# Kernel tuning notes

Hardware: AMD Instinct MI355X
Metric: run time of the kernel (lower is better)

The kernel has to match this reference:

```python
import jax, jax.numpy as jnp
import numpy as np
import math

D_MODEL = 1024
N_HEAD = 16
FFN_HIDDEN = 4096
EPS = 1e-12


def _layernorm(x, gamma, beta):
    # faithful to repo: unbiased std (ddof=1), divide by (std + eps)
    mean = jnp.mean(x, axis=-1, keepdims=True)
    std = jnp.std(x, axis=-1, keepdims=True, ddof=1)
    return gamma * ((x - mean) / (std + EPS)) + beta


def setup_inputs() -> dict:
    key = jax.random.key(0)
    ks = jax.random.split(key, 12)
    B, L, D, H = 2, 2048, D_MODEL, FFN_HIDDEN
    s = 0.02
    inp = {
        "x": jax.random.normal(ks[0], (B, L, D), dtype=jnp.float32),
        "src_mask": jnp.ones((B, 1, 1, L), dtype=jnp.int32),
        "wq_w": jax.random.normal(ks[1], (D, D), jnp.float32) * s,
        "wq_b": jnp.zeros((D,), jnp.float32),
        "wk_w": jax.random.normal(ks[2], (D, D), jnp.float32) * s,
        "wk_b": jnp.zeros((D,), jnp.float32),
        "wv_w": jax.random.normal(ks[3], (D, D), jnp.float32) * s,
        "wv_b": jnp.zeros((D,), jnp.float32),
        "wo_w": jax.random.normal(ks[4], (D, D), jnp.float32) * s,
        "wo_b": jnp.zeros((D,), jnp.float32),
        "gamma1": jnp.ones((D,), jnp.float32),
        "beta1": jnp.zeros((D,), jnp.float32),
        "ff1_w": jax.random.normal(ks[5], (D, H), jnp.float32) * s,
        "ff1_b": jnp.zeros((H,), jnp.float32),
        "ff2_w": jax.random.normal(ks[6], (H, D), jnp.float32) * s,
        "ff2_b": jnp.zeros((D,), jnp.float32),
        "gamma2": jnp.ones((D,), jnp.float32),
        "beta2": jnp.zeros((D,), jnp.float32),
    }
    return inp


def _encoder_layer(x, src_mask, wq_w, wq_b, wk_w, wk_b, wv_w, wv_b, wo_w, wo_b,
                   gamma1, beta1, ff1_w, ff1_b, ff2_w, ff2_b, gamma2, beta2):
    B, L, D = x.shape
    H = N_HEAD
    d_t = D // H
    # projections
    q = x @ wq_w + wq_b
    k = x @ wk_w + wk_b
    v = x @ wv_w + wv_b
    # faithful .view() split: reshape [B,L,D] -> [B,H,L,d_t] (no transpose)
    q = q.reshape(B, H, L, d_t)
    k = k.reshape(B, H, L, d_t)
    v = v.reshape(B, H, L, d_t)
    score = jnp.einsum("bhqd,bhkd->bhqk", q, k) / math.sqrt(d_t)
    score = jnp.where(src_mask == 0, jnp.float32(-1e-12), score)
    score = jax.nn.softmax(score, axis=-1)
    out = jnp.einsum("bhqk,bhkd->bhqd", score, v)
    out = out.reshape(B, L, D)  # faithful .view() concat
    attn = out @ wo_w + wo_b
    # residual + LN1 (dropout p=0)
    x1 = _layernorm(attn + x, gamma1, beta1)
    # FFN
    ff = jax.nn.relu(x1 @ ff1_w + ff1_b) @ ff2_w + ff2_b
    return _layernorm(ff + x1, gamma2, beta2)


def reference(x, src_mask, wq_w, wq_b, wk_w, wk_b, wv_w, wv_b, wo_w, wo_b,
              gamma1, beta1, ff1_w, ff1_b, ff2_w, ff2_b, gamma2, beta2):
    return _encoder_layer(x, src_mask, wq_w, wq_b, wk_w, wk_b, wv_w, wv_b,
                          wo_w, wo_b, gamma1, beta1, ff1_w, ff1_b, ff2_w,
                          ff2_b, gamma2, beta2)
```

## Files before the change

### kernel.cpp

```cpp
#include <hip/hip_runtime.h>
#include <hip/hip_bf16.h>
#include <cstdint>
#include <cstddef>

using bf16 = __hip_bfloat16;
typedef __attribute__((ext_vector_type(8))) short short8v;
typedef __attribute__((ext_vector_type(4))) short short4v;
typedef __attribute__((ext_vector_type(4))) float float4v;

__device__ inline float b2f(short s) {
  union { float f; uint32_t u; } z; z.u = ((uint32_t)(uint16_t)s) << 16; return z.f;
}
__device__ inline short f2b(float f) {
  bf16 h = __float2bfloat16(f);
  return *reinterpret_cast<short*>(&h);
}

typedef const __attribute__((address_space(1))) uint32_t* gas1p;
typedef __attribute__((address_space(3))) uint32_t* las3p;
__device__ inline void gload_lds16(const void* g, void* l) {
  __builtin_amdgcn_global_load_lds((gas1p)g, (las3p)l, 16, 0, 0);
}

__device__ inline void xcd_swizzle(int& bx, int& by, int& bz) {
  const int gx = gridDim.x, gy = gridDim.y;
  const int nwg = gx * gy * gridDim.z;
  const int wgid = blockIdx.x + gx * (blockIdx.y + gy * blockIdx.z);
  const int swz = (wgid & 7) * (nwg >> 3) + (wgid >> 3);
  bx = swz % gx;
  by = (swz / gx) % gy;
  bz = swz / (gx * gy);
}

__global__ __launch_bounds__(512, 2) void gemm_bt256(
    const bf16* __restrict__ A, const bf16* __restrict__ Bt,
    const float* __restrict__ bias, void* __restrict__ C,
    int K, int ldc, int relu_mode, int out_f32) {
  __shared__ __align__(16) bf16 As[256 * 32];
  __shared__ __align__(16) bf16 Bs[256 * 32];
  const int tid = threadIdx.x;
  const int w = tid >> 6, lane = tid & 63;
  const int quad = lane >> 4, l16 = lane & 15;
  const int wrow = (w >> 2) * 128, wcol = (w & 3) * 64;
  const int mbase = blockIdx.y * 256, nbase = blockIdx.x * 256;
  const int row0 = tid >> 2, p0 = tid & 3;
  const int row1 = (tid + 512) >> 2, p1 = (tid + 512) & 3;

  float4v acc[8][4];
#pragma unroll
  for (int i = 0; i < 8; i++)
#pragma unroll
    for (int j = 0; j < 4; j++) acc[i][j] = (float4v){0.f, 0.f, 0.f, 0.f};

  for (int k0 = 0; k0 < K; k0 += 32) {
    __syncthreads();
    gload_lds16(A + (size_t)(mbase + row0) * K + k0 + p0 * 8, (char*)As + w * 1024);
    gload_lds16(A + (size_t)(mbase + row1) * K + k0 + p1 * 8, (char*)As + 8192 + w * 1024);
    gload_lds16(Bt + (size_t)(nbase + row0) * K + k0 + p0 * 8, (char*)Bs + w * 1024);
    gload_lds16(Bt + (size_t)(nbase + row1) * K + k0 + p1 * 8, (char*)Bs + 8192 + w * 1024);
    __syncthreads();

    short8v a[8], b[4];
#pragma unroll
    for (int mt = 0; mt < 8; mt++)
      a[mt] = *reinterpret_cast<const short8v*>(As + (wrow + mt * 16 + l16) * 32 + quad * 8);
#pragma unroll
    for (int nt = 0; nt < 4; nt++)
      b[nt] = *reinterpret_cast<const short8v*>(Bs + (wcol + nt * 16 + l16) * 32 + quad * 8);
#pragma unroll
    for (int mt = 0; mt < 8; mt++)
#pragma unroll
      for (int nt = 0; nt < 4; nt++)
        acc[mt][nt] = __builtin_amdgcn_mfma_f32_16x16x32_bf16(a[mt], b[nt], acc[mt][nt], 0, 0, 0);
  }

#pragma unroll
  for (int nt = 0; nt < 4; nt++) {
    int col = nbase + wcol + nt * 16 + l16;
    float bv = bias[col];
#pragma unroll
    for (int mt = 0; mt < 8; mt++) {
      int row = mbase + wrow + mt * 16 + quad * 4;
#pragma unroll
      for (int r = 0; r < 4; r++) {
        float v = acc[mt][nt][r] + bv;
        if (relu_mode) v = fmaxf(v, 0.f);
        size_t idx = (size_t)(row + r) * ldc + col;
        if (out_f32) ((float*)C)[idx] = v;
        else         ((short*)C)[idx] = f2b(v);
      }
    }
  }
}

__global__ __launch_bounds__(256) void gemm_pipe(
    const bf16* __restrict__ A, const bf16* __restrict__ Bt,
    float* __restrict__ C, int K, int ldc, int k_len) {
  __shared__ __align__(16) bf16 As[2][2][128 * 32];
  __shared__ __align__(16) bf16 Bs[2][2][128 * 32];
  const int tid = threadIdx.x;
  const int w = tid >> 6, lane = tid & 63;
  const int quad = lane >> 4, l16 = lane & 15;
  const int wrow = (w >> 1) * 64, wcol = (w & 1) * 64;
  int bx, by, bz;
  xcd_swizzle(bx, by, bz);
  const int mbase = by * 128, nbase = bx * 128;
  const int c0 = w * 128 + lane;
  const int row0 = c0 >> 2, p0 = c0 & 3;
  const int row1 = (c0 + 64) >> 2, p1 = (c0 + 64) & 3;
  const int kbase = bz * k_len;

  const bf16* ag0 = A + (size_t)(mbase + row0) * K + kbase + p0 * 8;
  const bf16* ag1 = A + (size_t)(mbase + row1) * K + kbase + p1 * 8;
  const bf16* bg0 = Bt + (size_t)(nbase + row0) * K + kbase + p0 * 8;
  const bf16* bg1 = Bt + (size_t)(nbase + row1) * K + kbase + p1 * 8;

  auto stage = [&](int t64, int bi) {
    const int ko = t64 * 64;
#pragma unroll
    for (int h = 0; h < 2; h++) {
      char* da = (char*)As + (size_t)(bi * 2 + h) * 8192 + w * 2048;
      char* db = (char*)Bs + (size_t)(bi * 2 + h) * 8192 + w * 2048;
      gload_lds16(ag0 + ko + h * 32, da);
      gload_lds16(ag1 + ko + h * 32, da + 1024);
      gload_lds16(bg0 + ko + h * 32, db);
      gload_lds16(bg1 + ko + h * 32, db + 1024);
    }
  };

  float4v acc[4][4];
  for (int i = 0; i < 4; i++)
    for (int j = 0; j < 4; j++) acc[i][j] = (float4v){0.f, 0.f, 0.f, 0.f};

  const int KT2 = k_len >> 6;
  stage(0, 0);
  __syncthreads();

  for (int kt = 0; kt < KT2; kt++) {
    const int pb = kt & 1;
    if (kt + 1 < KT2) stage(kt + 1, 1 - pb);

#pragma unroll
    for (int h = 0; h < 2; h++) {
      const bf16* Ah = &As[pb][h][0];
      const bf16* Bh = &Bs[pb][h][0];
      short8v a[4], b[4];
      for (int mt = 0; mt < 4; mt++)
        a[mt] = *reinterpret_cast<const short8v*>(Ah + (wrow + mt * 16 + l16) * 32 + quad * 8);
      for (int nt = 0; nt < 4; nt++)
        b[nt] = *reinterpret_cast<const short8v*>(Bh + (wcol + nt * 16 + l16) * 32 + quad * 8);
      for (int mt = 0; mt < 4; mt++)
        for (int nt = 0; nt < 4; nt++)
          acc[mt][nt] = __builtin_amdgcn_mfma_f32_16x16x32_bf16(a[mt], b[nt], acc[mt][nt], 0, 0, 0);
    }

    __syncthreads();
  }

  for (int nt = 0; nt < 4; nt++) {
    int col = nbase + wcol + nt * 16 + l16;
    for (int mt = 0; mt < 4; mt++) {
      int row = mbase + wrow + mt * 16 + quad * 4;
      for (int r = 0; r < 4; r++)
        atomicAdd(&C[(size_t)(row + r) * ldc + col], acc[mt][nt][r]);
    }
  }
}

__global__ __launch_bounds__(256) void bias_init(
    const float* __restrict__ bias, float* __restrict__ C) {
  int c = threadIdx.x * 4;
  float4 bv = *reinterpret_cast<const float4*>(bias + c);
  *reinterpret_cast<float4*>(C + (size_t)blockIdx.x * 1024 + c) = bv;
}

__global__ __launch_bounds__(256) void attn_kernel(
    const bf16* __restrict__ qkv, const int* __restrict__ mask,
    bf16* __restrict__ ao) {
  __shared__ __align__(16) short Vt[2][64 * 72];
  __shared__ __align__(16) short Ks[2][64 * 64];

  const int tid = threadIdx.x;
  const int w = tid >> 6, lane = tid & 63;
  const int quad = lane >> 4, l16 = lane & 15;
  const int bh = blockIdx.y, b = bh >> 4;
  const int row0 = bh * 128;
  const int qbase = blockIdx.x * 128 + w * 32;
  const int kvp = tid & 15, dg = tid >> 4;
  const int krow = tid >> 3, kc = tid & 7;

  short8v aq[2][2];
  for (int h = 0; h < 2; h++)
    for (int dh = 0; dh < 2; dh++) {
      int local = (qbase + h * 16 + l16) * 64 + dh * 32 + quad * 8;
      aq[h][dh] = *reinterpret_cast<const short8v*>(
          qkv + (size_t)(row0 + (local >> 10)) * 3072 + (local & 1023));
    }

  const bf16* pks0;
  {
    int local = krow * 64 + kc * 8;
    pks0 = qkv + (size_t)(row0 + (local >> 10)) * 3072 + (local & 1023) + 1024;
  }
  const bf16* pks1 = pks0 + 6144;
  const bf16* pva;
  const bf16* pvb;
  {
    int la = (2 * kvp) * 64 + dg * 4;
    pva = qkv + (size_t)(row0 + (la >> 10)) * 3072 + (la & 1023) + 2048;
    int lb = (2 * kvp + 1) * 64 + dg * 4;
    pvb = qkv + (size_t)(row0 + (lb >> 10)) * 3072 + (lb & 1023) + 2048;
  }
  const bf16* pva2 = pva + 6144;
  const bf16* pvb2 = pvb + 6144;
  const int* pm = mask + b * 2048 + quad * 4;

  float4v o[2][4];
  for (int h = 0; h < 2; h++)
    for (int nt = 0; nt < 4; nt++) o[h][nt] = (float4v){0.f, 0.f, 0.f, 0.f};
  float4v lacc[2];
  lacc[0] = (float4v){0.f, 0.f, 0.f, 0.f};
  lacc[1] = (float4v){0.f, 0.f, 0.f, 0.f};
  short8v vone;
  for (int j = 0; j < 8; j++) vone[j] = (short)0x3F80;

  short8v kr0, kr1;
  short4v va, vb, va2, vb2;
  kr0 = *reinterpret_cast<const short8v*>(pks0);
  kr1 = *reinterpret_cast<const short8v*>(pks1);
  va  = *reinterpret_cast<const short4v*>(pva);
  vb  = *reinterpret_cast<const short4v*>(pvb);
  va2 = *reinterpret_cast<const short4v*>(pva2);
  vb2 = *reinterpret_cast<const short4v*>(pvb2);
  int4 mc0 = *reinterpret_cast<const int4*>(pm);
  int4 mc1 = *reinterpret_cast<const int4*>(pm + 16);
  int4 mc2 = *reinterpret_cast<const int4*>(pm + 32);
  int4 mc3 = *reinterpret_cast<const int4*>(pm + 48);
  pks0 += 12288; pks1 += 12288; pva += 12288; pvb += 12288;
  pva2 += 12288; pvb2 += 12288; pm += 64;
  {
    const int sw = (kc ^ (krow & 7)) << 3;
    *reinterpret_cast<short8v*>(&Ks[0][krow * 64 + sw]) = kr0;
    *reinterpret_cast<short8v*>(&Ks[0][(krow + 32) * 64 + sw]) = kr1;
    uint32_t* vt = reinterpret_cast<uint32_t*>(&Vt[0][0]);
    for (int i = 0; i < 4; i++) {
      vt[(dg * 4 + i) * 36 + kvp] =
          ((uint32_t)(uint16_t)vb[i] << 16) | (uint16_t)(uint16_t)va[i];
      vt[(dg * 4 + i) * 36 + 16 + kvp] =
          ((uint32_t)(uint16_t)vb2[i] << 16) | (uint16_t)(uint16_t)va2[i];
    }
  }
  __syncthreads();

  for (int it = 0; it < 32; it++) {
    const int pb = it & 1;
    short8v knr0, knr1;
    short4v vna, vnb, vna2, vnb2;
    int4 mn0, mn1, mn2, mn3;
    if (it < 31) {
      knr0 = *reinterpret_cast<const short8v*>(pks0);
      knr1 = *reinterpret_cast<const short8v*>(pks1);
      vna  = *reinterpret_cast<const short4v*>(pva);
      vnb  = *reinterpret_cast<const short4v*>(pvb);
      vna2 = *reinterpret_cast<const short4v*>(pva2);
      vnb2 = *reinterpret_cast<const short4v*>(pvb2);
      mn0 = *reinterpret_cast<const int4*>(pm);
      mn1 = *reinterpret_cast<const int4*>(pm + 16);
      mn2 = *reinterpret_cast<const int4*>(pm + 32);
      mn3 = *reinterpret_cast<const int4*>(pm + 48);
      pks0 += 12288; pks1 += 12288; pva += 12288; pvb += 12288;
      pva2 += 12288; pvb2 += 12288; pm += 64;
    }

#pragma unroll
    for (int sub = 0; sub < 2; sub++) {
      short8v kc_[2][2];
      for (int s = 0; s < 2; s++)
        for (int dh = 0; dh < 2; dh++) {
          int rr = sub * 32 + s * 16 + l16;
          kc_[s][dh] = *reinterpret_cast<const short8v*>(
              &Ks[pb][rr * 64 + (((dh * 4 + quad) ^ (l16 & 7)) << 3)]);
        }

      float4v st[2][2];
      for (int s = 0; s < 2; s++)
        for (int h = 0; h < 2; h++) {
          float4v t = (float4v){0.f, 0.f, 0.f, 0.f};
          t = __builtin_amdgcn_mfma_f32_16x16x32_bf16(kc_[s][0], aq[h][0], t, 0, 0, 0);
          t = __builtin_amdgcn_mfma_f32_16x16x32_bf16(kc_[s][1], aq[h][1], t, 0, 0, 0);
          st[s][h] = t;
        }

      short8v pf[2];
      for (int h = 0; h < 2; h++) {
        float ev[2][4];
        for (int s = 0; s < 2; s++) {
          int4 mv = sub ? (s ? mc3 : mc2) : (s ? mc1 : mc0);
          int mm[4] = {mv.x, mv.y, mv.z, mv.w};
          for (int r = 0; r < 4; r++) {
            float y = st[s][h][r];
            y = (mm[r] == 0) ? -1.4427e-12f : y;
            ev[s][r] = __builtin_amdgcn_exp2f(y);
          }
        }
        uint32_t a0, a1, b0, b1;
        asm("v_cvt_pk_bf16_f32 %0, %1, %2" : "=v"(a0) : "v"(ev[0][0]), "v"(ev[0][1]));
        asm("v_cvt_pk_bf16_f32 %0, %1, %2" : "=v"(a1) : "v"(ev[0][2]), "v"(ev[0][3]));
        asm("v_cvt_pk_bf16_f32 %0, %1, %2" : "=v"(b0) : "v"(ev[1][0]), "v"(ev[1][1]));
        asm("v_cvt_pk_bf16_f32 %0, %1, %2" : "=v"(b1) : "v"(ev[1][2]), "v"(ev[1][3]));
        asm("v_permlane32_swap_b32 %0, %1" : "+v"(b0), "+v"(a0));
        asm("v_permlane16_swap_b32 %0, %1" : "+v"(b0), "+v"(a0));
        asm("v_permlane32_swap_b32 %0, %1" : "+v"(b1), "+v"(a1));
        asm("v_permlane16_swap_b32 %0, %1" : "+v"(b1), "+v"(a1));
        union { short8v s8; uint32_t u[4]; } pfu;
        pfu.u[0] = a0; pfu.u[1] = a1; pfu.u[2] = b0; pfu.u[3] = b1;
        pf[h] = pfu.s8;
      }

      for (int h = 0; h < 2; h++)
        lacc[h] = __builtin_amdgcn_mfma_f32_16x16x32_bf16(pf[h], vone, lacc[h], 0, 0, 0);
      for (int nt = 0; nt < 4; nt++) {
        short8v bv = *reinterpret_cast<const short8v*>(
            &Vt[pb][(nt * 16 + l16) * 72 + sub * 32 + quad * 8]);
        for (int h = 0; h < 2; h++)
          o[h][nt] = __builtin_amdgcn_mfma_f32_16x16x32_bf16(pf[h], bv, o[h][nt], 0, 0, 0);
      }
    }

    if (it < 31) {
      const int sw = (kc ^ (krow & 7)) << 3;
      *reinterpret_cast<short8v*>(&Ks[1 - pb][krow * 64 + sw]) = knr0;
      *reinterpret_cast<short8v*>(&Ks[1 - pb][(krow + 32) * 64 + sw]) = knr1;
      uint32_t* vt = reinterpret_cast<uint32_t*>(&Vt[1 - pb][0]);
      for (int i = 0; i < 4; i++) {
        vt[(dg * 4 + i) * 36 + kvp] =
            ((uint32_t)(uint16_t)vnb[i] << 16) | (uint16_t)(uint16_t)vna[i];
        vt[(dg * 4 + i) * 36 + 16 + kvp] =
            ((uint32_t)(uint16_t)vnb2[i] << 16) | (uint16_t)(uint16_t)vna2[i];
      }
      mc0 = mn0; mc1 = mn1; mc2 = mn2; mc3 = mn3;
    }
    __syncthreads();
  }

  for (int h = 0; h < 2; h++)
    for (int r = 0; r < 4; r++) {
      float linv = 1.0f / lacc[h][r];
      int qg = qbase + h * 16 + quad * 4 + r;
      for (int nt = 0; nt < 4; nt++) {
        int d = nt * 16 + l16;
        ao[(size_t)bh * 131072 + (size_t)qg * 64 + d] = __float2bfloat16(o[h][nt][r] * linv);
      }
    }
}

__global__ __launch_bounds__(256) void ln_resid(
    const void* __restrict__ a, const void* __restrict__ xres,
    const float* __restrict__ gamma, const float* __restrict__ beta,
    void* __restrict__ out, int a_f32, int x_f32, int out_f32) {
  __shared__ float red[8];
  const int row = blockIdx.x, tid = threadIdx.x;
  const int w = tid >> 6, lane = tid & 63;
  const size_t base = (size_t)row * 1024;
  float v[4]; float sum = 0.f, ss = 0.f;
  for (int i = 0; i < 4; i++) {
    int c = tid + i * 256;
    float av = a_f32 ? ((const float*)a)[base + c] : b2f(((const short*)a)[base + c]);
    float xv = x_f32 ? ((const float*)xres)[base + c] : b2f(((const short*)xres)[base + c]);
    v[i] = av + xv;
    sum += v[i]; ss += v[i] * v[i];
  }
  for (int off = 1; off < 64; off <<= 1) {
    sum += __shfl_xor(sum, off);
    ss  += __shfl_xor(ss, off);
  }
  if (lane == 0) { red[w * 2] = sum; red[w * 2 + 1] = ss; }
  __syncthreads();
  sum = red[0] + red[2] + red[4] + red[6];
  ss  = red[1] + red[3] + red[5] + red[7];
  float mean = sum * (1.0f / 1024.0f);
  float var = (ss - 1024.0f * mean * mean) * (1.0f / 1023.0f);
  var = fmaxf(var, 0.f);
  float rden = 1.0f / (sqrtf(var) + 1e-12f);
  for (int i = 0; i < 4; i++) {
    int c = tid + i * 256;
    float y = gamma[c] * ((v[i] - mean) * rden) + beta[c];
    if (out_f32) ((float*)out)[base + c] = y;
    else         ((short*)out)[base + c] = f2b(y);
  }
}

__global__ __launch_bounds__(256) void transpose_k(
    const float* __restrict__ in, bf16* __restrict__ out, int R, int C,
    float scale) {
  __shared__ short t[32][33];
  const int tx = threadIdx.x, ty = threadIdx.y;
  const int cb = blockIdx.x * 32, rb = blockIdx.y * 32;
  for (int j = 0; j < 4; j++)
    t[ty + j * 8][tx] = f2b(in[(size_t)(rb + ty + j * 8) * C + cb + tx] * scale);
  __syncthreads();
  for (int j = 0; j < 4; j++)
    ((short*)out)[(size_t)(cb + ty + j * 8) * R + rb + tx] = t[tx][ty + j * 8];
}

__global__ __launch_bounds__(256) void concat3(
    const float* __restrict__ a, const float* __restrict__ b,
    const float* __restrict__ c, float* __restrict__ out) {
  int i = blockIdx.x * 256 + threadIdx.x;
  float v;
  if (i < 1024)       v = a[i] * 0.18033688f;
  else if (i < 2048)  v = b[i - 1024];
  else                v = c[i - 2048];
  out[i] = v;
}

__global__ __launch_bounds__(256) void cast_f32_bf16(
    const float* __restrict__ in, bf16* __restrict__ out) {
  int i0 = (blockIdx.x * 256 + threadIdx.x) * 4;
  float4 f = *reinterpret_cast<const float4*>(in + i0);
  short* o = (short*)out + i0;
  o[0] = f2b(f.x); o[1] = f2b(f.y); o[2] = f2b(f.z); o[3] = f2b(f.w);
}

extern "C" void kernel_launch(void* const* d_in, const int* in_sizes, int n_in,
                              void* d_out, int out_size, void* d_ws, size_t ws_size,
                              hipStream_t stream) {
  (void)in_sizes; (void)n_in; (void)out_size; (void)ws_size;
  const float* x    = (const float*)d_in[0];
  const int*   mask = (const int*)d_in[1];
  const float* wq_w = (const float*)d_in[2];
  const float* wq_b = (const float*)d_in[3];
  const float* wk_w = (const float*)d_in[4];
  const float* wk_b = (const float*)d_in[5];
  const float* wv_w = (const float*)d_in[6];
  const float* wv_b = (const float*)d_in[7];
  const float* wo_w = (const float*)d_in[8];
  const float* wo_b = (const float*)d_in[9];
  const float* g1   = (const float*)d_in[10];
  const float* be1  = (const float*)d_in[11];
  const float* f1w  = (const float*)d_in[12];
  const float* f1b  = (const float*)d_in[13];
  const float* f2w  = (const float*)d_in[14];
  const float* f2b_ = (const float*)d_in[15];
  const float* g2   = (const float*)d_in[16];
  const float* be2  = (const float*)d_in[17];
  float* out = (float*)d_out;
  char* ws = (char*)d_ws;

  bf16*  QKV  = (bf16*)(ws + 0);
  bf16*  Xbf  = (bf16*)(ws + 25165824);
  bf16*  AO   = (bf16*)(ws + 25165824);
  float* PROJ = (float*)(ws + 0);
  bf16*  H    = (bf16*)(ws + 0);
  bf16*  X1   = (bf16*)(ws + 33554432);
  bf16*  WT   = (bf16*)(ws + 41943040);
  float* BQKV = (float*)(ws + 48234496);

  const float QSCALE = 0.18033688f;

  dim3 tb(32, 8);
  cast_f32_bf16<<<dim3(4096), dim3(256), 0, stream>>>(x, Xbf);
  transpose_k<<<dim3(32, 32), tb, 0, stream>>>(wq_w, WT, 1024, 1024, QSCALE);
  transpose_k<<<dim3(32, 32), tb, 0, stream>>>(wk_w, WT + 1024 * 1024, 1024, 1024, 1.0f);
  transpose_k<<<dim3(32, 32), tb, 0, stream>>>(wv_w, WT + 2 * 1024 * 1024, 1024, 1024, 1.0f);
  concat3<<<dim3(12), dim3(256), 0, stream>>>(wq_b, wk_b, wv_b, BQKV);
  gemm_bt256<<<dim3(12, 16), dim3(512), 0, stream>>>(Xbf, WT, BQKV, QKV, 1024, 3072, 0, 0);
  attn_kernel<<<dim3(16, 32), dim3(256), 0, stream>>>(QKV, mask, AO);
  transpose_k<<<dim3(32, 32), tb, 0, stream>>>(wo_w, WT, 1024, 1024, 1.0f);
  bias_init<<<dim3(4096), dim3(256), 0, stream>>>(wo_b, PROJ);
  gemm_pipe<<<dim3(8, 32, 2), dim3(256), 0, stream>>>(AO, WT, PROJ, 1024, 1024, 512);
  ln_resid<<<dim3(4096), dim3(256), 0, stream>>>(PROJ, x, g1, be1, X1, 1, 1, 0);
  transpose_k<<<dim3(128, 32), tb, 0, stream>>>(f1w, WT, 1024, 4096, 1.0f);
  gemm_bt256<<<dim3(16, 16), dim3(512), 0, stream>>>(X1, WT, f1b, H, 1024, 4096, 1, 0);
  transpose_k<<<dim3(32, 128), tb, 0, stream>>>(f2w, WT, 4096, 1024, 1.0f);
  bias_init<<<dim3(4096), dim3(256), 0, stream>>>(f2b_, out);
  gemm_pipe<<<dim3(8, 32, 2), dim3(256), 0, stream>>>(H, WT, out, 4096, 1024, 2048);
  ln_resid<<<dim3(4096), dim3(256), 0, stream>>>(out, X1, g2, be2, out, 1, 0, 1);
}
```

Measured before the change: 432.6 us.

## Double-buffer GEMM LDS tiles with K=64 stages to overlap loads and MFMA

The 256x256 GEMM kernel now uses two LDS buffers, each holding a 64-wide K slab split into two 32-wide halves. It prefetches the next slab with global_load_lds while computing on the current one, and needs one barrier per 64 K instead of two per 32 K. LDS use grows from 32KB to 128KB per block, which may cap occupancy below the declared 2 blocks per CU. The code also assumes K is a multiple of 64.

```diff
diff --git a/kernel.cpp b/kernel.cpp
--- a/kernel.cpp
+++ b/kernel.cpp
@@ -36,8 +36,8 @@
     const bf16* __restrict__ A, const bf16* __restrict__ Bt,
     const float* __restrict__ bias, void* __restrict__ C,
     int K, int ldc, int relu_mode, int out_f32) {
-  __shared__ __align__(16) bf16 As[256 * 32];
-  __shared__ __align__(16) bf16 Bs[256 * 32];
+  __shared__ __align__(16) bf16 As[2][2][256 * 32];
+  __shared__ __align__(16) bf16 Bs[2][2][256 * 32];
   const int tid = threadIdx.x;
   const int w = tid >> 6, lane = tid & 63;
   const int quad = lane >> 4, l16 = lane & 15;
@@ -46,32 +46,57 @@
   const int row0 = tid >> 2, p0 = tid & 3;
   const int row1 = (tid + 512) >> 2, p1 = (tid + 512) & 3;
 
+  const bf16* ag0 = A + (size_t)(mbase + row0) * K + p0 * 8;
+  const bf16* ag1 = A + (size_t)(mbase + row1) * K + p1 * 8;
+  const bf16* bg0 = Bt + (size_t)(nbase + row0) * K + p0 * 8;
+  const bf16* bg1 = Bt + (size_t)(nbase + row1) * K + p1 * 8;
+
+  auto stage = [&](int t64, int bi) {
+    const int ko = t64 * 64;
+#pragma unroll
+    for (int h = 0; h < 2; h++) {
+      char* da = (char*)As + (size_t)(bi * 2 + h) * 16384 + w * 1024;
+      char* db = (char*)Bs + (size_t)(bi * 2 + h) * 16384 + w * 1024;
+      gload_lds16(ag0 + ko + h * 32, da);
+      gload_lds16(ag1 + ko + h * 32, da + 8192);
+      gload_lds16(bg0 + ko + h * 32, db);
+      gload_lds16(bg1 + ko + h * 32, db + 8192);
+    }
+  };
+
   float4v acc[8][4];
 #pragma unroll
   for (int i = 0; i < 8; i++)
 #pragma unroll
     for (int j = 0; j < 4; j++) acc[i][j] = (float4v){0.f, 0.f, 0.f, 0.f};
 
-  for (int k0 = 0; k0 < K; k0 += 32) {
+  const int KT2 = K >> 6;
+  stage(0, 0);
+  __syncthreads();
+
+  for (int kt = 0; kt < KT2; kt++) {
+    const int pb = kt & 1;
+    if (kt + 1 < KT2) stage(kt + 1, 1 - pb);
+
+#pragma unroll
+    for (int h = 0; h < 2; h++) {
+      const bf16* Ah = &As[pb][h][0];
+      const bf16* Bh = &Bs[pb][h][0];
+      short8v a[8], b[4];
+#pragma unroll
+      for (int mt = 0; mt < 8; mt++)
+        a[mt] = *reinterpret_cast<const short8v*>(Ah + (wrow + mt * 16 + l16) * 32 + quad * 8);
+#pragma unroll
+      for (int nt = 0; nt < 4; nt++)
+        b[nt] = *reinterpret_cast<const short8v*>(Bh + (wcol + nt * 16 + l16) * 32 + quad * 8);
+#pragma unroll
+      for (int mt = 0; mt < 8; mt++)
+#pragma unroll
+        for (int nt = 0; nt < 4; nt++)
+          acc[mt][nt] = __builtin_amdgcn_mfma_f32_16x16x32_bf16(a[mt], b[nt], acc[mt][nt], 0, 0, 0);
+    }
+
     __syncthreads();
-    gload_lds16(A + (size_t)(mbase + row0) * K + k0 + p0 * 8, (char*)As + w * 1024);
-    gload_lds16(A + (size_t)(mbase + row1) * K + k0 + p1 * 8, (char*)As + 8192 + w * 1024);
-    gload_lds16(Bt + (size_t)(nbase + row0) * K + k0 + p0 * 8, (char*)Bs + w * 1024);
-    gload_lds16(Bt + (size_t)(nbase + row1) * K + k0 + p1 * 8, (char*)Bs + 8192 + w * 1024);
-    __syncthreads();
-
-    short8v a[8], b[4];
-#pragma unroll
-    for (int mt = 0; mt < 8; mt++)
-      a[mt] = *reinterpret_cast<const short8v*>(As + (wrow + mt * 16 + l16) * 32 + quad * 8);
-#pragma unroll
-    for (int nt = 0; nt < 4; nt++)
-      b[nt] = *reinterpret_cast<const short8v*>(Bs + (wcol + nt * 16 + l16) * 32 + quad * 8);
-#pragma unroll
-    for (int mt = 0; mt < 8; mt++)
-#pragma unroll
-      for (int nt = 0; nt < 4; nt++)
-        acc[mt][nt] = __builtin_amdgcn_mfma_f32_16x16x32_bf16(a[mt], b[nt], acc[mt][nt], 0, 0, 0);
   }
 
 #pragma unroll
```

After: 421.6 us. 1.03x faster.
